# Performance work log

Measured on AMD Instinct MI355X. Metric: run time of the kernel, lower is better.

The kernel has to match this reference:

```python
import jax, jax.numpy as jnp
import numpy as np

B, T, S, U, VOCAB = 32, 64, 64, 512, 65


def setup_inputs() -> dict:
    key = jax.random.key(0)
    ks = jax.random.split(key, 16)
    sd = 0.05
    return {
        "shifted_labels": jax.random.randint(ks[0], (B, T), 0, VOCAB),
        "encoder_output": jax.random.normal(ks[1], (B, S, U), jnp.float32),
        "enc_state_h": jax.random.normal(ks[2], (B, U), jnp.float32),
        "enc_state_c": jax.random.normal(ks[3], (B, U), jnp.float32),
        # decoder LSTM params (keras gate order i,f,g,o)
        "Wx": jax.random.normal(ks[4], (VOCAB, 4 * U), jnp.float32) * sd,
        "Wh": jax.random.normal(ks[5], (U, 4 * U), jnp.float32) * sd,
        "b": jnp.zeros((4 * U,), jnp.float32),
        # Bahdanau attention params
        "W1": jax.random.normal(ks[6], (U, U), jnp.float32) * sd,
        "b1": jnp.zeros((U,), jnp.float32),
        "W2": jax.random.normal(ks[7], (U, U), jnp.float32) * sd,
        "b2": jnp.zeros((U,), jnp.float32),
        "V": jax.random.normal(ks[8], (U, 1), jnp.float32) * sd,
        "bv": jnp.zeros((1,), jnp.float32),
    }


def _lstm(xz, h0, c0, Wh):
    # xz: [B, T, 4U] precomputed input projections
    def step(carry, xz_t):
        h, c = carry
        z = xz_t + h @ Wh
        i, f, g, o = jnp.split(z, 4, axis=-1)
        c = jax.nn.sigmoid(f) * c + jax.nn.sigmoid(i) * jnp.tanh(g)
        h = jax.nn.sigmoid(o) * jnp.tanh(c)
        return (h, c), h

    (_, _), hs = jax.lax.scan(step, (h0, c0), jnp.swapaxes(xz, 0, 1))
    return jnp.swapaxes(hs, 0, 1)  # [B, T, U]


def reference(shifted_labels, encoder_output, enc_state_h, enc_state_c,
              Wx, Wh, b, W1, b1, W2, b2, V, bv):
    vocab = Wx.shape[0]
    x = jax.nn.one_hot(shifted_labels, vocab, dtype=encoder_output.dtype)  # [B,T,vocab]
    xz = jnp.einsum('btv,vk->btk', x, Wx) + b                              # [B,T,4U]
    dec = _lstm(xz, enc_state_h, enc_state_c, Wh)                          # [B,T,U]
    # Bahdanau attention, vectorized over all decoder timesteps at once
    d1 = dec @ W1 + b1                # [B,T,U]
    e2 = encoder_output @ W2 + b2     # [B,S,U]  (computed once, not per step)
    score = jnp.tanh(d1[:, :, None, :] + e2[:, None, :, :]) @ V + bv  # [B,T,S,1]
    w = jax.nn.softmax(score[..., 0], axis=-1)  # softmax over encoder positions S
    return jnp.transpose(w, (0, 2, 1))          # [B,S,T] (stack axis=2 in original)
```

## Files before the change

### kernel.cpp

```cpp
#include <hip/hip_runtime.h>
#include <hip/hip_bf16.h>


#define NB 32
#define NT 64
#define NS 64
#define NU 512
#define N4U 2048
#define NV 65
#define NWG 32

typedef unsigned int u32;
typedef __bf16 bf16_t;
typedef bf16_t bf16x8 __attribute__((ext_vector_type(8)));
typedef float f32x4 __attribute__((ext_vector_type(4)));
typedef u32 u32x4 __attribute__((ext_vector_type(4)));
typedef u32 u32x2 __attribute__((ext_vector_type(2)));

__device__ __forceinline__ unsigned short f2bf(float f) {
  u32 u = __builtin_bit_cast(u32, f);
  u += 0x7fffu + ((u >> 16) & 1u);
  return (unsigned short)(u >> 16);
}
__device__ __forceinline__ float bf2f(unsigned short s) {
  return __builtin_bit_cast(float, (u32)s << 16);
}
__device__ __forceinline__ u32 pk2(float a, float b) {
  return (u32)f2bf(a) | ((u32)f2bf(b) << 16);
}
__device__ __forceinline__ float sigf(float x) { return 1.0f / (1.0f + __expf(-x)); }
__device__ __forceinline__ float tanhfast(float x) {
  float e = __expf(2.0f * x);
  return 1.0f - 2.0f / (e + 1.0f);
}

__global__ __launch_bounds__(256, 1)
void lstm_kernel(const int* __restrict__ labels,
                 const float* __restrict__ h0,
                 const float* __restrict__ c0,
                 const float* __restrict__ Wx,
                 const float* __restrict__ Wh,
                 const float* __restrict__ bias,
                 u32* __restrict__ hbuf2,
                 u32* __restrict__ dec_u)
{
  __shared__ float z_buf[NB][65];
  __shared__ float c_lds[NB][16];
  __shared__ float wx_lds[NV][65];
  __shared__ unsigned char lab_lds[NB * NT];
  __shared__ __align__(16) u32 hx[2][2][64][36];

  const int tid  = threadIdx.x;
  const int g    = blockIdx.x;
  const int wave = tid >> 6, lane = tid & 63;
  const int wm   = wave >> 1, wn = wave & 1;
  const int l15  = lane & 15, l4 = lane >> 4;

  for (int i = tid; i < NV * 64; i += 256) {
    int v = i >> 6, c = i & 63;
    int j = (c >> 4) * NU + g * 16 + (c & 15);
    wx_lds[v][c] = Wx[v * N4U + j] + bias[j];
  }
  for (int i = tid; i < NB * 16; i += 256) {
    int r = i >> 4, u = i & 15;
    c_lds[r][u] = c0[r * NU + g * 16 + u];
  }
  for (int i = tid; i < NB * NT; i += 256) lab_lds[i] = (unsigned char)labels[i];

  bf16x8 bfrag[16][2];
#pragma unroll
  for (int kt = 0; kt < 16; ++kt) {
#pragma unroll
    for (int nt = 0; nt < 2; ++nt) {
      int c = wn * 32 + nt * 16 + l15;
      int j = (c >> 4) * NU + g * 16 + (c & 15);
      int kb = kt * 32 + l4 * 8;
      union { unsigned short us[8]; bf16x8 v; } bu;
#pragma unroll
      for (int e = 0; e < 8; ++e) bu.us[e] = f2bf(Wh[(kb + e) * N4U + j]);
      bfrag[kt][nt] = bu.v;
    }
  }

  const int arow = wm * 16 + l15;
  u32x4 afrag[16];
#pragma unroll
  for (int kt = 0; kt < 16; ++kt) {
    const float* hp = h0 + arow * NU + kt * 32 + l4 * 8;
    u32x4 t;
    t.x = pk2(hp[0], hp[1]); t.y = pk2(hp[2], hp[3]);
    t.z = pk2(hp[4], hp[5]); t.w = pk2(hp[6], hp[7]);
    afrag[kt] = t;
  }

  const int bb = tid >> 3;
  const int u2 = (tid & 7) * 2;
  const int ci = g * 8 + (tid & 7);

  for (int s = 0; s < NT; ++s) {
    f32x4 a00 = {0.f,0.f,0.f,0.f}, a01 = a00, a10 = a00, a11 = a00;
#pragma unroll
    for (int kt = 0; kt < 16; kt += 2) {
      bf16x8 av0 = __builtin_bit_cast(bf16x8, afrag[kt]);
      bf16x8 av1 = __builtin_bit_cast(bf16x8, afrag[kt + 1]);
      a00 = __builtin_amdgcn_mfma_f32_16x16x32_bf16(av0, bfrag[kt][0],     a00, 0, 0, 0);
      a10 = __builtin_amdgcn_mfma_f32_16x16x32_bf16(av0, bfrag[kt][1],     a10, 0, 0, 0);
      a01 = __builtin_amdgcn_mfma_f32_16x16x32_bf16(av1, bfrag[kt + 1][0], a01, 0, 0, 0);
      a11 = __builtin_amdgcn_mfma_f32_16x16x32_bf16(av1, bfrag[kt + 1][1], a11, 0, 0, 0);
    }
    f32x4 acc0 = a00 + a01, acc1 = a10 + a11;

#pragma unroll
    for (int ri = 0; ri < 4; ++ri) {
      z_buf[wm * 16 + l4 * 4 + ri][wn * 32 + l15]      = acc0[ri];
      z_buf[wm * 16 + l4 * 4 + ri][wn * 32 + 16 + l15] = acc1[ri];
    }
    __syncthreads();

    int lab = lab_lds[bb * NT + s];
    float hv[2];
#pragma unroll
    for (int q = 0; q < 2; ++q) {
      int u = u2 + q;
      float zi = z_buf[bb][u]      + wx_lds[lab][u];
      float zf = z_buf[bb][16 + u] + wx_lds[lab][16 + u];
      float zg = z_buf[bb][32 + u] + wx_lds[lab][32 + u];
      float zo = z_buf[bb][48 + u] + wx_lds[lab][48 + u];
      float cc = sigf(zf) * c_lds[bb][u] + sigf(zi) * tanhfast(zg);
      c_lds[bb][u] = cc;
      hv[q] = sigf(zo) * tanhfast(cc);
    }
    u32 pkv = pk2(hv[0], hv[1]);
    dec_u[(bb * NT + s) * 256 + ci] = pkv;

    if (s == NT - 1) break;

    {
      u32x2 v2; v2.x = pkv; v2.y = (u32)(s + 1);
      u32* sp = hbuf2 + (((s + 1) & 1) << 14) + bb * 512 + ci * 2;
      asm volatile("global_store_dwordx2 %0, %1, off sc0 sc1"
                   :: "v"(sp), "v"(v2) : "memory");
    }

    u32x4 t[16];
    {
      const u32* qp = hbuf2 + (((s + 1) & 1) << 14) + arow * 512
                      + wn * 256 + l4 * 8;
      const u32 tg = (u32)(s + 1);
      int guard = 0;
      for (;;) {
        asm volatile(
          "global_load_dwordx4 %0, %16, off sc0 sc1\n\t"
          "global_load_dwordx4 %1, %16, off offset:16 sc0 sc1\n\t"
          "global_load_dwordx4 %2, %16, off offset:128 sc0 sc1\n\t"
          "global_load_dwordx4 %3, %16, off offset:144 sc0 sc1\n\t"
          "global_load_dwordx4 %4, %16, off offset:256 sc0 sc1\n\t"
          "global_load_dwordx4 %5, %16, off offset:272 sc0 sc1\n\t"
          "global_load_dwordx4 %6, %16, off offset:384 sc0 sc1\n\t"
          "global_load_dwordx4 %7, %16, off offset:400 sc0 sc1\n\t"
          "global_load_dwordx4 %8, %16, off offset:512 sc0 sc1\n\t"
          "global_load_dwordx4 %9, %16, off offset:528 sc0 sc1\n\t"
          "global_load_dwordx4 %10, %16, off offset:640 sc0 sc1\n\t"
          "global_load_dwordx4 %11, %16, off offset:656 sc0 sc1\n\t"
          "global_load_dwordx4 %12, %16, off offset:768 sc0 sc1\n\t"
          "global_load_dwordx4 %13, %16, off offset:784 sc0 sc1\n\t"
          "global_load_dwordx4 %14, %16, off offset:896 sc0 sc1\n\t"
          "global_load_dwordx4 %15, %16, off offset:912 sc0 sc1\n\t"
          "s_waitcnt vmcnt(0)"
          : "=&v"(t[0]),  "=&v"(t[1]),  "=&v"(t[2]),  "=&v"(t[3]),
            "=&v"(t[4]),  "=&v"(t[5]),  "=&v"(t[6]),  "=&v"(t[7]),
            "=&v"(t[8]),  "=&v"(t[9]),  "=&v"(t[10]), "=&v"(t[11]),
            "=&v"(t[12]), "=&v"(t[13]), "=&v"(t[14]), "=&v"(t[15])
          : "v"(qp)
          : "memory");
        bool ok = true;
#pragma unroll
        for (int i = 0; i < 16; ++i)
          ok = ok && (t[i].y == tg) && (t[i].w == tg);
        if (__all(ok)) break;
        if (++guard > 100000) break;
        __builtin_amdgcn_s_sleep(1);
      }
    }

    {
      u32* hw = &hx[wm][wn][lane][0];
#pragma unroll
      for (int j = 0; j < 8; ++j) {
        u32x4 d; d.x = t[2*j].x; d.y = t[2*j].z; d.z = t[2*j+1].x; d.w = t[2*j+1].z;
        *reinterpret_cast<u32x4*>(hw + j * 4) = d;
        if (wn == 0) afrag[j] = d; else afrag[8 + j] = d;
      }
      __syncthreads();
      const u32* hr = &hx[wm][wn ^ 1][lane][0];
#pragma unroll
      for (int j = 0; j < 8; ++j) {
        u32x4 d = *reinterpret_cast<const u32x4*>(hr + j * 4);
        if (wn == 0) afrag[8 + j] = d; else afrag[j] = d;
      }
    }
  }
}

__global__ __launch_bounds__(256, 1)
void proj_kernel(const u32* __restrict__ dec_u,
                 const float* __restrict__ enc,
                 const float* __restrict__ W1,
                 const float* __restrict__ b1,
                 const float* __restrict__ W2,
                 const float* __restrict__ b2,
                 unsigned short* __restrict__ d1_bf,
                 unsigned short* __restrict__ e2_bf)
{
  const int tid = threadIdx.x;
  const int wave = tid >> 6, lane = tid & 63;
  const int l15 = lane & 15, l4 = lane >> 4;
  const int w  = blockIdx.x * 4 + wave;
  const int rt = w >> 3, cg = w & 7;
  const bool isdec = (rt < 128);
  const int r0 = (isdec ? rt : rt - 128) * 16;
  const float* Wm  = isdec ? W1 : W2;
  const float* bv_ = isdec ? b1 : b2;
  unsigned short* outp = isdec ? d1_bf : e2_bf;

  f32x4 acc[4] = {};
  const int arow = r0 + l15;
  for (int kt = 0; kt < 16; ++kt) {
    int k0 = kt * 32 + l4 * 8;
    bf16x8 a;
    if (isdec) {
      a = __builtin_bit_cast(bf16x8,
            *reinterpret_cast<const uint4*>(dec_u + arow * 256 + (k0 >> 1)));
    } else {
      const float* ep = enc + arow * NU + k0;
      union { unsigned short us[8]; bf16x8 v; } au;
#pragma unroll
      for (int e = 0; e < 8; ++e) au.us[e] = f2bf(ep[e]);
      a = au.v;
    }
#pragma unroll
    for (int nt = 0; nt < 4; ++nt) {
      int col = cg * 64 + nt * 16 + l15;
      union { unsigned short us[8]; bf16x8 v; } bu;
#pragma unroll
      for (int e = 0; e < 8; ++e) bu.us[e] = f2bf(Wm[(k0 + e) * NU + col]);
      acc[nt] = __builtin_amdgcn_mfma_f32_16x16x32_bf16(a, bu.v, acc[nt], 0, 0, 0);
    }
  }
#pragma unroll
  for (int nt = 0; nt < 4; ++nt) {
    int col = cg * 64 + nt * 16 + l15;
    float bc = bv_[col];
#pragma unroll
    for (int ri = 0; ri < 4; ++ri) {
      int row = r0 + l4 * 4 + ri;
      outp[row * NU + col] = f2bf(acc[nt][ri] + bc);
    }
  }
}

__global__ __launch_bounds__(256, 1)
void score_kernel(const unsigned short* __restrict__ d1_bf,
                  const unsigned short* __restrict__ e2_bf,
                  const float* __restrict__ V,
                  float* __restrict__ out)
{
  const int tid = threadIdx.x;
  const int wave = tid >> 6, lane = tid & 63;
  const int p = blockIdx.x * 4 + wave;
  const int bb = p >> 6, t = p & 63;

  union { uint4 q; unsigned short us[8]; } dv;
  dv.q = *reinterpret_cast<const uint4*>(d1_bf + (bb * 64 + t) * NU + lane * 8);
  float d1f[8], Vf[8];
#pragma unroll
  for (int e = 0; e < 8; ++e) { d1f[e] = bf2f(dv.us[e]); Vf[e] = V[lane * 8 + e]; }

  float sc = 0.f;
  for (int s = 0; s < NS; ++s) {
    union { uint4 q; unsigned short us[8]; } ev;
    ev.q = *reinterpret_cast<const uint4*>(e2_bf + (bb * 64 + s) * NU + lane * 8);
    float part = 0.f;
#pragma unroll
    for (int e = 0; e < 8; ++e) part += tanhfast(d1f[e] + bf2f(ev.us[e])) * Vf[e];
#pragma unroll
    for (int o = 32; o > 0; o >>= 1) part += __shfl_xor(part, o);
    sc = (lane == s) ? part : sc;
  }
  float m = sc;
#pragma unroll
  for (int o = 32; o > 0; o >>= 1) m = fmaxf(m, __shfl_xor(m, o));
  float ex = __expf(sc - m);
  float sum = ex;
#pragma unroll
  for (int o = 32; o > 0; o >>= 1) sum += __shfl_xor(sum, o);
  out[(bb * 64 + lane) * 64 + t] = ex / sum;
}

extern "C" void kernel_launch(void* const* d_in, const int* in_sizes, int n_in,
                              void* d_out, int out_size, void* d_ws, size_t ws_size,
                              hipStream_t stream)
{
  (void)in_sizes; (void)n_in; (void)out_size;
  const int*   labels = (const int*)  d_in[0];
  const float* enc    = (const float*)d_in[1];
  const float* h0     = (const float*)d_in[2];
  const float* c0     = (const float*)d_in[3];
  const float* Wx     = (const float*)d_in[4];
  const float* Wh     = (const float*)d_in[5];
  const float* bias   = (const float*)d_in[6];
  const float* W1     = (const float*)d_in[7];
  const float* b1     = (const float*)d_in[8];
  const float* W2     = (const float*)d_in[9];
  const float* b2     = (const float*)d_in[10];
  const float* V      = (const float*)d_in[11];

  char* ws = (char*)d_ws;
  const size_t OFS_HB2 = 1024;
  const size_t OFS_DEC = OFS_HB2 + (1u << 18);
  const size_t OFS_D1  = OFS_DEC + (2u << 20);
  const size_t OFS_E2  = OFS_D1  + (2u << 20);
  if (ws_size < OFS_E2 + (2u << 20)) return;

  u32* hbuf2 = (u32*)(ws + OFS_HB2);
  u32* dec_u = (u32*)(ws + OFS_DEC);
  unsigned short* d1_bf = (unsigned short*)(ws + OFS_D1);
  unsigned short* e2_bf = (unsigned short*)(ws + OFS_E2);
  float* out = (float*)d_out;

  lstm_kernel<<<dim3(NWG), dim3(256), 0, stream>>>(labels, h0, c0, Wx, Wh, bias,
                                                   hbuf2, dec_u);
  proj_kernel<<<dim3(512), dim3(256), 0, stream>>>(dec_u, enc, W1, b1, W2, b2,
                                                   d1_bf, e2_bf);
  score_kernel<<<dim3(512), dim3(256), 0, stream>>>(d1_bf, e2_bf, V, out);
}
```

Baseline: 440.2 us.

## Overlap encoder projection with LSTM recurrence and add lightweight flag polling

Adds 32 extra workgroups to the LSTM launch that compute e2 = enc@W2+b2 while the 32 recurrent workgroups run. This hides the encoder projection behind the latency-bound sequential LSTM, and proj_kernel shrinks to handle only the decoder projection. It also adds a cheap three-load readiness poll before the full 16-load fetch of the hidden state, and lowers the guard count on that fetch loop. One risk is that the extra workgroups compete for memory bandwidth or for CU placement with the spin-waiting LSTM workgroups.

```diff
diff --git a/kernel.cpp b/kernel.cpp
--- a/kernel.cpp
+++ b/kernel.cpp
@@ -41,8 +41,12 @@
                  const float* __restrict__ Wx,
                  const float* __restrict__ Wh,
                  const float* __restrict__ bias,
+                 const float* __restrict__ enc,
+                 const float* __restrict__ W2,
+                 const float* __restrict__ b2,
                  u32* __restrict__ hbuf2,
-                 u32* __restrict__ dec_u)
+                 u32* __restrict__ dec_u,
+                 unsigned short* __restrict__ e2_bf)
 {
   __shared__ float z_buf[NB][65];
   __shared__ float c_lds[NB][16];
@@ -53,8 +57,47 @@
   const int tid  = threadIdx.x;
   const int g    = blockIdx.x;
   const int wave = tid >> 6, lane = tid & 63;
-  const int wm   = wave >> 1, wn = wave & 1;
   const int l15  = lane & 15, l4 = lane >> 4;
+
+  if (g >= NWG) {
+    const int r0 = (g - NWG) * 64 + wave * 16;
+    const int arowE = r0 + l15;
+    u32x4 afragE[16];
+#pragma unroll
+    for (int kt = 0; kt < 16; ++kt) {
+      const float* ep = enc + arowE * NU + kt * 32 + l4 * 8;
+      u32x4 t;
+      t.x = pk2(ep[0], ep[1]); t.y = pk2(ep[2], ep[3]);
+      t.z = pk2(ep[4], ep[5]); t.w = pk2(ep[6], ep[7]);
+      afragE[kt] = t;
+    }
+    for (int cg = 0; cg < 8; ++cg) {
+      f32x4 acc[4] = {};
+      for (int kt = 0; kt < 16; ++kt) {
+        bf16x8 a = __builtin_bit_cast(bf16x8, afragE[kt]);
+        int k0 = kt * 32 + l4 * 8;
+#pragma unroll
+        for (int nt = 0; nt < 4; ++nt) {
+          int col = cg * 64 + nt * 16 + l15;
+          union { unsigned short us[8]; bf16x8 v; } bu;
+#pragma unroll
+          for (int e = 0; e < 8; ++e) bu.us[e] = f2bf(W2[(k0 + e) * NU + col]);
+          acc[nt] = __builtin_amdgcn_mfma_f32_16x16x32_bf16(a, bu.v, acc[nt], 0, 0, 0);
+        }
+      }
+#pragma unroll
+      for (int nt = 0; nt < 4; ++nt) {
+        int col = cg * 64 + nt * 16 + l15;
+        float bc = b2[col];
+#pragma unroll
+        for (int ri = 0; ri < 4; ++ri)
+          e2_bf[(r0 + l4 * 4 + ri) * NU + col] = f2bf(acc[nt][ri] + bc);
+      }
+    }
+    return;
+  }
+
+  const int wm = wave >> 1, wn = wave & 1;
 
   for (int i = tid; i < NV * 64; i += 256) {
     int v = i >> 6, c = i & 63;
@@ -142,11 +185,29 @@
                    :: "v"(sp), "v"(v2) : "memory");
     }
 
+    const u32* qp = hbuf2 + (((s + 1) & 1) << 14) + arow * 512
+                    + wn * 256 + l4 * 8;
+    const u32 tg = (u32)(s + 1);
+
+    {
+      int guard = 0;
+      for (;;) {
+        u32x2 s0, s1, s2;
+        asm volatile(
+          "global_load_dwordx2 %0, %3, off sc0 sc1\n\t"
+          "global_load_dwordx2 %1, %3, off offset:456 sc0 sc1\n\t"
+          "global_load_dwordx2 %2, %3, off offset:920 sc0 sc1\n\t"
+          "s_waitcnt vmcnt(0)"
+          : "=&v"(s0), "=&v"(s1), "=&v"(s2)
+          : "v"(qp) : "memory");
+        if (__all(s0.y == tg && s1.y == tg && s2.y == tg)) break;
+        if (++guard > 200000) break;
+        __builtin_amdgcn_s_sleep(1);
+      }
+    }
+
     u32x4 t[16];
     {
-      const u32* qp = hbuf2 + (((s + 1) & 1) << 14) + arow * 512
-                      + wn * 256 + l4 * 8;
-      const u32 tg = (u32)(s + 1);
       int guard = 0;
       for (;;) {
         asm volatile(
@@ -178,7 +239,7 @@
         for (int i = 0; i < 16; ++i)
           ok = ok && (t[i].y == tg) && (t[i].w == tg);
         if (__all(ok)) break;
-        if (++guard > 100000) break;
+        if (++guard > 20000) break;
         __builtin_amdgcn_s_sleep(1);
       }
     }
@@ -204,57 +265,40 @@
 
 __global__ __launch_bounds__(256, 1)
 void proj_kernel(const u32* __restrict__ dec_u,
-                 const float* __restrict__ enc,
                  const float* __restrict__ W1,
                  const float* __restrict__ b1,
-                 const float* __restrict__ W2,
-                 const float* __restrict__ b2,
-                 unsigned short* __restrict__ d1_bf,
-                 unsigned short* __restrict__ e2_bf)
+                 unsigned short* __restrict__ d1_bf)
 {
   const int tid = threadIdx.x;
   const int wave = tid >> 6, lane = tid & 63;
   const int l15 = lane & 15, l4 = lane >> 4;
   const int w  = blockIdx.x * 4 + wave;
   const int rt = w >> 3, cg = w & 7;
-  const bool isdec = (rt < 128);
-  const int r0 = (isdec ? rt : rt - 128) * 16;
-  const float* Wm  = isdec ? W1 : W2;
-  const float* bv_ = isdec ? b1 : b2;
-  unsigned short* outp = isdec ? d1_bf : e2_bf;
+  const int r0 = rt * 16;
 
   f32x4 acc[4] = {};
   const int arow = r0 + l15;
   for (int kt = 0; kt < 16; ++kt) {
     int k0 = kt * 32 + l4 * 8;
-    bf16x8 a;
-    if (isdec) {
-      a = __builtin_bit_cast(bf16x8,
-            *reinterpret_cast<const uint4*>(dec_u + arow * 256 + (k0 >> 1)));
-    } else {
-      const float* ep = enc + arow * NU + k0;
-      union { unsigned short us[8]; bf16x8 v; } au;
-#pragma unroll
-      for (int e = 0; e < 8; ++e) au.us[e] = f2bf(ep[e]);
-      a = au.v;
-    }
+    bf16x8 a = __builtin_bit_cast(bf16x8,
+          *reinterpret_cast<const uint4*>(dec_u + arow * 256 + (k0 >> 1)));
 #pragma unroll
     for (int nt = 0; nt < 4; ++nt) {
       int col = cg * 64 + nt * 16 + l15;
       union { unsigned short us[8]; bf16x8 v; } bu;
 #pragma unroll
-      for (int e = 0; e < 8; ++e) bu.us[e] = f2bf(Wm[(k0 + e) * NU + col]);
+      for (int e = 0; e < 8; ++e) bu.us[e] = f2bf(W1[(k0 + e) * NU + col]);
       acc[nt] = __builtin_amdgcn_mfma_f32_16x16x32_bf16(a, bu.v, acc[nt], 0, 0, 0);
     }
   }
 #pragma unroll
   for (int nt = 0; nt < 4; ++nt) {
     int col = cg * 64 + nt * 16 + l15;
-    float bc = bv_[col];
+    float bc = b1[col];
 #pragma unroll
     for (int ri = 0; ri < 4; ++ri) {
       int row = r0 + l4 * 4 + ri;
-      outp[row * NU + col] = f2bf(acc[nt][ri] + bc);
+      d1_bf[row * NU + col] = f2bf(acc[nt][ri] + bc);
     }
   }
 }
@@ -328,9 +372,9 @@
   unsigned short* e2_bf = (unsigned short*)(ws + OFS_E2);
   float* out = (float*)d_out;
 
-  lstm_kernel<<<dim3(NWG), dim3(256), 0, stream>>>(labels, h0, c0, Wx, Wh, bias,
-                                                   hbuf2, dec_u);
-  proj_kernel<<<dim3(512), dim3(256), 0, stream>>>(dec_u, enc, W1, b1, W2, b2,
-                                                   d1_bf, e2_bf);
+  lstm_kernel<<<dim3(2 * NWG), dim3(256), 0, stream>>>(labels, h0, c0, Wx, Wh,
+                                                       bias, enc, W2, b2,
+                                                       hbuf2, dec_u, e2_bf);
+  proj_kernel<<<dim3(256), dim3(256), 0, stream>>>(dec_u, W1, b1, d1_bf);
   score_kernel<<<dim3(512), dim3(256), 0, stream>>>(d1_bf, e2_bf, V, out);
 }
```

Measured after the change: 428.5 us. 2.7% less time.
